# Kernel optimization log

Measured on AMD Instinct MI355X. Metric: run time of the kernel, lower is better.

## Reference

```python
import jax, jax.numpy as jnp
import numpy as np

N_NODES = 100000
N_EDGES = 1600000
N_GRAPHS = 256
NEG_SLOPE_GAT = 0.2   # GATConv default
NEG_SLOPE_ACT = 0.01  # F.leaky_relu default


def _leaky(x, s):
    return jnp.where(x >= 0, x, s * x)


def _gat_layer(x, src, dst, W, a_src, a_dst, b, n):
    # h = W x ; per-node attention logits
    h = x @ W                      # [N, D]
    al_s = h @ a_src               # [N]
    al_d = h @ a_dst               # [N]
    e = _leaky(al_s[src] + al_d[dst], NEG_SLOPE_GAT)  # [E]
    # segment softmax over incoming edges of each dst node
    m = jax.ops.segment_max(e, dst, num_segments=n)
    m = jnp.where(jnp.isfinite(m), m, 0.0)
    ex = jnp.exp(e - m[dst])
    s = jax.ops.segment_sum(ex, dst, num_segments=n)
    alpha = ex / (s[dst] + 1e-16)
    out = jax.ops.segment_sum(h[src] * alpha[:, None], dst, num_segments=n)
    return out + b


def setup_inputs() -> dict:
    key = jax.random.key(0)
    ks = jax.random.split(key, 12)
    x = jax.random.normal(ks[0], (N_NODES, 72), dtype=jnp.float32)
    edge_index = jax.random.randint(ks[1], (2, N_EDGES), 0, N_NODES, dtype=jnp.int64)
    batch = jnp.sort(jax.random.randint(ks[2], (N_NODES,), 0, N_GRAPHS, dtype=jnp.int64))
    def glorot(k, shape):
        fan = shape[0] + shape[-1]
        return jax.random.normal(k, shape, dtype=jnp.float32) * jnp.sqrt(2.0 / fan)
    return {
        "x": x, "edge_index": edge_index, "batch": batch,
        "W1": glorot(ks[3], (72, 64)),
        "a_src1": glorot(ks[4], (64,)), "a_dst1": glorot(ks[5], (64,)),
        "b1": jnp.zeros((64,), jnp.float32),
        "W2": glorot(ks[6], (64, 64)),
        "a_src2": glorot(ks[7], (64,)), "a_dst2": glorot(ks[8], (64,)),
        "b2": jnp.zeros((64,), jnp.float32),
        "fcW": glorot(ks[9], (64, 2)),
        "fcb": jnp.zeros((2,), jnp.float32),
    }


def reference(x, edge_index, batch, W1, a_src1, a_dst1, b1, W2, a_src2, a_dst2, b2, fcW, fcb):
    n = x.shape[0]
    # PyG GATConv adds self-loops by default
    loops = jnp.arange(n, dtype=edge_index.dtype)
    src = jnp.concatenate([edge_index[0], loops])
    dst = jnp.concatenate([edge_index[1], loops])
    h = _gat_layer(x, src, dst, W1, a_src1, a_dst1, b1, n)
    h = _leaky(h, NEG_SLOPE_ACT)
    h = _gat_layer(h, src, dst, W2, a_src2, a_dst2, b2, n)
    # global mean pool over graphs
    sums = jax.ops.segment_sum(h, batch, num_segments=N_GRAPHS)
    cnt = jax.ops.segment_sum(jnp.ones((n,), h.dtype), batch, num_segments=N_GRAPHS)
    pooled = sums / jnp.maximum(cnt, 1.0)[:, None]
    # dropout is identity at inference
    return pooled @ fcW + fcb
```

## Files before the change

### kernel.cpp

```cpp
#include <hip/hip_runtime.h>
#include <hip/hip_bf16.h>
#include <math.h>


#define NPB 256
#define EPB 4096
#define PSTRIDE 4608
#define XPAD 68

__device__ __forceinline__ unsigned int f2bf(float v) {
    unsigned int b = __float_as_uint(v);
    b += 0x7FFFu + ((b >> 16) & 1u);
    return b >> 16;
}

__device__ __forceinline__ int scanIncl256(int v, int t, int* wsum) {
    int lane = t & 63, wv = t >> 6;
#pragma unroll
    for (int o = 1; o < 64; o <<= 1) {
        int u = __shfl_up(v, o);
        if (lane >= o) v += u;
    }
    if (lane == 63) wsum[wv] = v;
    __syncthreads();
    int base = 0;
#pragma unroll
    for (int i = 0; i < 3; i++) base += (i < wv) ? wsum[i] : 0;
    __syncthreads();
    return v + base;
}

struct PartSh {
    int h[512];
    int ls[512];
    int lcur[512];
    int hb[512];
    int s2[256];
    int wsum[4];
    unsigned int Qp[EPB];
    unsigned short Bq[EPB];
};
struct GemmSh {
    float Ws[72 * 64];
    float xs[72][XPAD];
};
union FusedSh { PartSh p; GemmSh g; };

__global__ __launch_bounds__(256) void part_gemm(const int* __restrict__ ei,
                                                 int E, int NB,
                                                 int* __restrict__ bcur,
                                                 unsigned int* __restrict__ pairs,
                                                 int gPart,
                                                 const float* __restrict__ x,
                                                 const float* __restrict__ W,
                                                 const float* __restrict__ a_src,
                                                 const float* __restrict__ a_dst,
                                                 unsigned short* __restrict__ h16,
                                                 float* __restrict__ al_s,
                                                 float* __restrict__ al_d,
                                                 int n) {
    __shared__ FusedSh sh;
    int t = threadIdx.x;
    if ((int)blockIdx.x < gPart) {
        int* h = sh.p.h;
        int* ls = sh.p.ls;
        int* lcur = sh.p.lcur;
        int* hb = sh.p.hb;
        int* s2 = sh.p.s2;
        for (int i = t; i < 512; i += 256) h[i] = 0;
        __syncthreads();
        int i0 = blockIdx.x * EPB;
        unsigned int val[16];
        int bk[16];
        const int4* s4p = (const int4*)(ei);
        const int4* d4p = (const int4*)(ei + E);
#pragma unroll
        for (int k = 0; k < 4; k++) {
            int vbase = (i0 >> 2) + k * 256 + t;
            int i = vbase << 2;
            if (i < E) {
                int4 s4 = s4p[vbase];
                int4 d4 = d4p[vbase];
                int ss[4] = {s4.x, s4.y, s4.z, s4.w};
                int dd[4] = {d4.x, d4.y, d4.z, d4.w};
#pragma unroll
                for (int j = 0; j < 4; j++) {
                    int e = k * 4 + j;
                    bk[e] = dd[j] >> 8;
                    val[e] = (unsigned)ss[j] | ((unsigned)(dd[j] & 255) << 24);
                    atomicAdd(&h[bk[e]], 1);
                }
            } else {
#pragma unroll
                for (int j = 0; j < 4; j++) bk[k * 4 + j] = -1;
            }
        }
        __syncthreads();
        int p0 = h[2 * t], p1 = h[2 * t + 1];
        int incl = scanIncl256(p0 + p1, t, sh.p.wsum);
        s2[t] = incl;
        int ex = incl - p0 - p1;
        ls[2 * t] = ex;           ls[2 * t + 1] = ex + p0;
        lcur[2 * t] = ex;         lcur[2 * t + 1] = ex + p0;
        __syncthreads();
        for (int b = t; b < NB; b += 256)
            hb[b] = h[b] ? atomicAdd(&bcur[b], h[b]) : 0;
        __syncthreads();
#pragma unroll
        for (int e = 0; e < 16; e++) {
            if (bk[e] < 0) continue;
            int pos = atomicAdd(&lcur[bk[e]], 1);
            sh.p.Qp[pos] = val[e];
            sh.p.Bq[pos] = (unsigned short)bk[e];
        }
        __syncthreads();
        int total = s2[255];
        for (int j = t; j < total; j += 256) {
            int bkj = sh.p.Bq[j];
            int gp = hb[bkj] + (j - ls[bkj]);
            if (gp < PSTRIDE)
                pairs[(size_t)bkj * PSTRIDE + gp] = sh.p.Qp[j];
        }
    } else {
        constexpr int IN_DIM = 72;
        float* Ws = sh.g.Ws;
        int nbase = ((int)blockIdx.x - gPart) * 64;

        for (int idx = t; idx < IN_DIM * 16; idx += 256)
            ((float4*)Ws)[idx] = ((const float4*)W)[idx];
        const float* xb = x + (size_t)nbase * IN_DIM;
        int lim = min(64, n - nbase) * IN_DIM;
        constexpr int NV = (64 * IN_DIM) / 4;
        for (int idx = t; idx < NV; idx += 256) {
            int f0 = idx * 4;
            float4 v = make_float4(0.0f, 0.0f, 0.0f, 0.0f);
            if (f0 < lim) v = ((const float4*)xb)[idx];
            int node = f0 / IN_DIM;
            int k = f0 - node * IN_DIM;
            sh.g.xs[k + 0][node] = v.x;
            sh.g.xs[k + 1][node] = v.y;
            sh.g.xs[k + 2][node] = v.z;
            sh.g.xs[k + 3][node] = v.w;
        }
        __syncthreads();

        int cg = t & 15;
        int ng = t >> 4;
        float acc[4][4] = {};
#pragma unroll 8
        for (int k = 0; k < IN_DIM; k++) {
            float4 xv = *(const float4*)&sh.g.xs[k][ng * 4];
            float4 wv = *(const float4*)&Ws[k * 64 + cg * 4];
            float xa[4] = {xv.x, xv.y, xv.z, xv.w};
            float wa[4] = {wv.x, wv.y, wv.z, wv.w};
#pragma unroll
            for (int i = 0; i < 4; i++)
#pragma unroll
                for (int j = 0; j < 4; j++)
                    acc[i][j] += xa[i] * wa[j];
        }

        float4 as4 = *(const float4*)(a_src + cg * 4);
        float4 ad4 = *(const float4*)(a_dst + cg * 4);
#pragma unroll
        for (int i = 0; i < 4; i++) {
            int node = nbase + ng * 4 + i;
            if (node < n) {
                uint2 p;
                p.x = f2bf(acc[i][0]) | (f2bf(acc[i][1]) << 16);
                p.y = f2bf(acc[i][2]) | (f2bf(acc[i][3]) << 16);
                *(uint2*)(h16 + (size_t)node * 64 + cg * 4) = p;
            }
            float vs = acc[i][0] * as4.x + acc[i][1] * as4.y +
                       acc[i][2] * as4.z + acc[i][3] * as4.w;
            float vd = acc[i][0] * ad4.x + acc[i][1] * ad4.y +
                       acc[i][2] * ad4.z + acc[i][3] * ad4.w;
#pragma unroll
            for (int o = 8; o; o >>= 1) {
                vs += __shfl_xor(vs, o);
                vd += __shfl_xor(vd, o);
            }
            if (cg == 0 && node < n) { al_s[node] = vs; al_d[node] = vd; }
        }
    }
}

__global__ __launch_bounds__(256) void build_csr(const unsigned int* __restrict__ pairs,
                                                 const int* __restrict__ bcur,
                                                 int n, int NB,
                                                 int* __restrict__ rowptr,
                                                 int* __restrict__ srcs) {
    int b = blockIdx.x, t = threadIdx.x;
    __shared__ int c[512];
    __shared__ int s2[256];
    __shared__ int wsum[4];
    __shared__ int sbase, stot;
    __shared__ unsigned int Q[PSTRIDE];
    __shared__ int S[NPB + PSTRIDE];
    __shared__ int hist[256];
    __shared__ int hcur[256];
    int c0 = (2 * t < NB) ? min(bcur[2 * t], PSTRIDE) : 0;
    int c1 = (2 * t + 1 < NB) ? min(bcur[2 * t + 1], PSTRIDE) : 0;
    c[2 * t] = c0; c[2 * t + 1] = c1;
    hist[t] = 0;
    __syncthreads();
    int incl = scanIncl256(c0 + c1, t, wsum);
    s2[t] = incl;
    __syncthreads();
    if (t == 0) {
        int p = b >> 1;
        int ex = s2[p] - (c[2 * p] + c[2 * p + 1]);
        sbase = ex + ((b & 1) ? c[b & ~1] : 0);
        stot = s2[255];
    }
    __syncthreads();
    int d0 = b << 8;
    int nb = min(NPB, n - d0);
    int cnt_b = c[b];
    int csr0 = sbase + d0;
    const unsigned int* pb = pairs + (size_t)b * PSTRIDE;

    for (int j = t; j < cnt_b; j += 256)
        atomicAdd(&hist[(pb[j] & 0xFFFFFFu) >> 9], 1);
    __syncthreads();
    int hv = hist[t];
    int hincl = scanIncl256(hv, t, wsum);
    hcur[t] = hincl - hv;
    __syncthreads();
    for (int j = t; j < cnt_b; j += 256) {
        unsigned int p = pb[j];
        int pos = atomicAdd(&hcur[(p & 0xFFFFFFu) >> 9], 1);
        Q[pos] = p;
    }
    __syncthreads();

    __shared__ int deg[NPB];
    __shared__ int cur[NPB];
    deg[t] = (t < nb) ? 1 : 0;
    __syncthreads();
    for (int j = t; j < cnt_b; j += 256)
        atomicAdd(&deg[Q[j] >> 24], 1);
    __syncthreads();
    int v = deg[t];
    int dincl = scanIncl256(v, t, wsum);
    int excl = dincl - v;
    if (t < nb) {
        rowptr[d0 + t] = csr0 + excl;
        S[excl] = d0 + t;
        cur[t] = excl + 1;
    }
    __syncthreads();
    for (int j = t; j < cnt_b; j += 256) {
        unsigned int p = Q[j];
        int off = atomicAdd(&cur[p >> 24], 1);
        S[off] = (int)(p & 0x00FFFFFFu);
    }
    __syncthreads();
    int seg = nb + cnt_b;
    for (int j = t; j < seg; j += 256)
        srcs[csr0 + j] = S[j];
    if (b == 0 && t == 0) rowptr[n] = n + stot;
}

template <int IN_DIM>
__global__ __launch_bounds__(256) void node_gemm(const float* __restrict__ x,
                                                 const float* __restrict__ W,
                                                 const float* __restrict__ a_src,
                                                 const float* __restrict__ a_dst,
                                                 const float* __restrict__ bias_in,
                                                 float slope_in,
                                                 unsigned short* __restrict__ h16,
                                                 float* __restrict__ al_s,
                                                 float* __restrict__ al_d,
                                                 int n) {
    __shared__ float Ws[IN_DIM * 64];
    __shared__ float xs[IN_DIM][XPAD];
    int t = threadIdx.x;
    int nbase = blockIdx.x * 64;

    for (int idx = t; idx < IN_DIM * 16; idx += 256)
        ((float4*)Ws)[idx] = ((const float4*)W)[idx];
    const float* xb = x + (size_t)nbase * IN_DIM;
    int lim = min(64, n - nbase) * IN_DIM;
    constexpr int NV = (64 * IN_DIM) / 4;
    for (int idx = t; idx < NV; idx += 256) {
        int f0 = idx * 4;
        float4 v = make_float4(0.0f, 0.0f, 0.0f, 0.0f);
        if (f0 < lim) v = ((const float4*)xb)[idx];
        int node = f0 / IN_DIM;
        int k = f0 - node * IN_DIM;
        if (bias_in) {
            v.x += bias_in[k + 0];
            v.y += bias_in[k + 1];
            v.z += bias_in[k + 2];
            v.w += bias_in[k + 3];
            v.x = (v.x >= 0.0f) ? v.x : slope_in * v.x;
            v.y = (v.y >= 0.0f) ? v.y : slope_in * v.y;
            v.z = (v.z >= 0.0f) ? v.z : slope_in * v.z;
            v.w = (v.w >= 0.0f) ? v.w : slope_in * v.w;
        }
        xs[k + 0][node] = v.x;
        xs[k + 1][node] = v.y;
        xs[k + 2][node] = v.z;
        xs[k + 3][node] = v.w;
    }
    __syncthreads();

    int cg = t & 15;
    int ng = t >> 4;
    float acc[4][4] = {};
#pragma unroll 8
    for (int k = 0; k < IN_DIM; k++) {
        float4 xv = *(const float4*)&xs[k][ng * 4];
        float4 wv = *(const float4*)&Ws[k * 64 + cg * 4];
        float xa[4] = {xv.x, xv.y, xv.z, xv.w};
        float wa[4] = {wv.x, wv.y, wv.z, wv.w};
#pragma unroll
        for (int i = 0; i < 4; i++)
#pragma unroll
            for (int j = 0; j < 4; j++)
                acc[i][j] += xa[i] * wa[j];
    }

    float4 as4 = *(const float4*)(a_src + cg * 4);
    float4 ad4 = *(const float4*)(a_dst + cg * 4);
#pragma unroll
    for (int i = 0; i < 4; i++) {
        int node = nbase + ng * 4 + i;
        if (node < n) {
            uint2 p;
            p.x = f2bf(acc[i][0]) | (f2bf(acc[i][1]) << 16);
            p.y = f2bf(acc[i][2]) | (f2bf(acc[i][3]) << 16);
            *(uint2*)(h16 + (size_t)node * 64 + cg * 4) = p;
        }
        float vs = acc[i][0] * as4.x + acc[i][1] * as4.y +
                   acc[i][2] * as4.z + acc[i][3] * as4.w;
        float vd = acc[i][0] * ad4.x + acc[i][1] * ad4.y +
                   acc[i][2] * ad4.z + acc[i][3] * ad4.w;
#pragma unroll
        for (int o = 8; o; o >>= 1) {
            vs += __shfl_xor(vs, o);
            vd += __shfl_xor(vd, o);
        }
        if (cg == 0 && node < n) { al_s[node] = vs; al_d[node] = vd; }
    }
}

__device__ __forceinline__ void bf8_fma(float* acc, uint4 q, float w) {
    acc[0] += w * __uint_as_float(q.x << 16);
    acc[1] += w * __uint_as_float(q.x & 0xFFFF0000u);
    acc[2] += w * __uint_as_float(q.y << 16);
    acc[3] += w * __uint_as_float(q.y & 0xFFFF0000u);
    acc[4] += w * __uint_as_float(q.z << 16);
    acc[5] += w * __uint_as_float(q.z & 0xFFFF0000u);
    acc[6] += w * __uint_as_float(q.w << 16);
    acc[7] += w * __uint_as_float(q.w & 0xFFFF0000u);
}

__global__ __launch_bounds__(256) void gat_aggregate(const int* __restrict__ rowptr,
                                                     const int* __restrict__ srcs,
                                                     const float* __restrict__ als,
                                                     const float* __restrict__ ald,
                                                     const unsigned short* __restrict__ h16,
                                                     float* __restrict__ hout,
                                                     int n) {
    int t = threadIdx.x;
    int sub = t >> 3, lane = t & 7;
    int node = blockIdx.x * 32 + sub;
    if (node >= n) return;
    int beg = rowptr[node], end = rowptr[node + 1];
    float aldv = ald[node];
    const unsigned short* hb = h16 + lane * 8;

    float acc[8] = {};
    float sm = 0.0f;
    int j = beg;
    if (j + 4 <= end) {
        int s0 = srcs[j], s1 = srcs[j + 1], s2 = srcs[j + 2], s3 = srcs[j + 3];
        for (; j + 8 <= end; j += 4) {
            int n0 = srcs[j + 4], n1 = srcs[j + 5];
            int n2 = srcs[j + 6], n3 = srcs[j + 7];
            float e0 = als[s0] + aldv, e1 = als[s1] + aldv;
            float e2 = als[s2] + aldv, e3 = als[s3] + aldv;
            uint4 q0 = *(const uint4*)(hb + (size_t)s0 * 64);
            uint4 q1 = *(const uint4*)(hb + (size_t)s1 * 64);
            uint4 q2 = *(const uint4*)(hb + (size_t)s2 * 64);
            uint4 q3 = *(const uint4*)(hb + (size_t)s3 * 64);
            e0 = (e0 >= 0.0f) ? e0 : 0.2f * e0;
            e1 = (e1 >= 0.0f) ? e1 : 0.2f * e1;
            e2 = (e2 >= 0.0f) ? e2 : 0.2f * e2;
            e3 = (e3 >= 0.0f) ? e3 : 0.2f * e3;
            float w0 = __expf(e0), w1 = __expf(e1);
            float w2 = __expf(e2), w3 = __expf(e3);
            sm += (w0 + w1) + (w2 + w3);
            bf8_fma(acc, q0, w0);
            bf8_fma(acc, q1, w1);
            bf8_fma(acc, q2, w2);
            bf8_fma(acc, q3, w3);
            s0 = n0; s1 = n1; s2 = n2; s3 = n3;
        }
        {
            float e0 = als[s0] + aldv, e1 = als[s1] + aldv;
            float e2 = als[s2] + aldv, e3 = als[s3] + aldv;
            uint4 q0 = *(const uint4*)(hb + (size_t)s0 * 64);
            uint4 q1 = *(const uint4*)(hb + (size_t)s1 * 64);
            uint4 q2 = *(const uint4*)(hb + (size_t)s2 * 64);
            uint4 q3 = *(const uint4*)(hb + (size_t)s3 * 64);
            e0 = (e0 >= 0.0f) ? e0 : 0.2f * e0;
            e1 = (e1 >= 0.0f) ? e1 : 0.2f * e1;
            e2 = (e2 >= 0.0f) ? e2 : 0.2f * e2;
            e3 = (e3 >= 0.0f) ? e3 : 0.2f * e3;
            float w0 = __expf(e0), w1 = __expf(e1);
            float w2 = __expf(e2), w3 = __expf(e3);
            sm += (w0 + w1) + (w2 + w3);
            bf8_fma(acc, q0, w0);
            bf8_fma(acc, q1, w1);
            bf8_fma(acc, q2, w2);
            bf8_fma(acc, q3, w3);
            j += 4;
        }
    }
    for (; j < end; j++) {
        int s = srcs[j];
        float e = als[s] + aldv;
        e = (e >= 0.0f) ? e : 0.2f * e;
        float w = __expf(e);
        uint4 q = *(const uint4*)(hb + (size_t)s * 64);
        sm += w;
        bf8_fma(acc, q, w);
    }

    float inv = 1.0f / (sm + 1e-16f);
    float4 o0 = make_float4(acc[0] * inv, acc[1] * inv, acc[2] * inv, acc[3] * inv);
    float4 o1 = make_float4(acc[4] * inv, acc[5] * inv, acc[6] * inv, acc[7] * inv);
    float* op = hout + (size_t)node * 64 + lane * 8;
    *(float4*)op = o0;
    *(float4*)(op + 4) = o1;
}

__global__ __launch_bounds__(256) void pool_fc(const float* __restrict__ hout,
                                               const float* __restrict__ b2,
                                               const int* __restrict__ batch,
                                               const float* __restrict__ fcW,
                                               const float* __restrict__ fcb,
                                               float* __restrict__ out, int n) {
    int g = blockIdx.x;
    int t = threadIdx.x;
    __shared__ int sLo, sHi;
    __shared__ float red[16][64];
    if (t == 0) {
        int lo = 0, hi = n;
        while (lo < hi) { int m = (lo + hi) >> 1; if (batch[m] < g) lo = m + 1; else hi = m; }
        sLo = lo;
    } else if (t == 64) {
        int lo = 0, hi = n;
        while (lo < hi) { int m = (lo + hi) >> 1; if (batch[m] < g + 1) lo = m + 1; else hi = m; }
        sHi = lo;
    }
    __syncthreads();
    int lo = sLo, hi = sHi;
    int q = t & 15;
    int r = t >> 4;
    float4 a4 = make_float4(0.0f, 0.0f, 0.0f, 0.0f);
    for (int node = lo + r; node < hi; node += 16) {
        float4 v = *(const float4*)(hout + (size_t)node * 64 + q * 4);
        a4.x += v.x; a4.y += v.y; a4.z += v.z; a4.w += v.w;
    }
    *(float4*)&red[r][q * 4] = a4;
    __syncthreads();
    if (t < 64) {
        float c = (float)(hi - lo);
        float s = 0.0f;
#pragma unroll
        for (int i = 0; i < 16; i++) s += red[i][t];
        s += c * b2[t];
        float cd = (c > 1.0f) ? c : 1.0f;
        float p = s / cd;
        float s0 = p * fcW[t * 2 + 0];
        float s1 = p * fcW[t * 2 + 1];
#pragma unroll
        for (int o = 32; o; o >>= 1) {
            s0 += __shfl_xor(s0, o);
            s1 += __shfl_xor(s1, o);
        }
        if (t == 0) {
            out[g * 2 + 0] = s0 + fcb[0];
            out[g * 2 + 1] = s1 + fcb[1];
        }
    }
}

extern "C" void kernel_launch(void* const* d_in, const int* in_sizes, int n_in,
                              void* d_out, int out_size, void* d_ws, size_t ws_size,
                              hipStream_t stream) {
    const float* x    = (const float*)d_in[0];
    const int*   ei   = (const int*)d_in[1];
    const int*   batch= (const int*)d_in[2];
    const float* W1   = (const float*)d_in[3];
    const float* as1  = (const float*)d_in[4];
    const float* ad1  = (const float*)d_in[5];
    const float* b1   = (const float*)d_in[6];
    const float* W2   = (const float*)d_in[7];
    const float* as2  = (const float*)d_in[8];
    const float* ad2  = (const float*)d_in[9];
    const float* b2   = (const float*)d_in[10];
    const float* fcW  = (const float*)d_in[11];
    const float* fcb  = (const float*)d_in[12];
    float* out = (float*)d_out;

    const int N = in_sizes[2];
    const int E = in_sizes[1] / 2;
    const int G = out_size / 2;
    const int tot = E + N;
    const int NB = (N + NPB - 1) / NPB;

    float* ws     = (float*)d_ws;
    float* bufO   = ws;
    unsigned int* pairs  = (unsigned int*)bufO;
    float* als    = bufO + (size_t)N * 64;
    float* ald    = als + N;
    int*   rowptr = (int*)(ald + N);
    int*   srcs   = rowptr + N + 1;
    int*   bcur   = srcs + tot;
    unsigned short* bufH16 = (unsigned short*)(bcur + NB);

    dim3 b256(256);
    int gPart = (E + EPB - 1) / EPB;
    int gGemm = (N + 63) / 64;
    int gAgg  = (N + 31) / 32;

    hipMemsetAsync(bcur, 0, (size_t)NB * sizeof(int), stream);
    part_gemm<<<gPart + gGemm, b256, 0, stream>>>(ei, E, NB, bcur, pairs, gPart,
                                                  x, W1, as1, ad1,
                                                  bufH16, als, ald, N);
    build_csr<<<NB, b256, 0, stream>>>(pairs, bcur, N, NB, rowptr, srcs);

    gat_aggregate<<<gAgg, b256, 0, stream>>>(rowptr, srcs, als, ald, bufH16, bufO, N);

    node_gemm<64><<<gGemm, b256, 0, stream>>>(bufO, W2, as2, ad2, b1, 0.01f,
                                              bufH16, als, ald, N);
    gat_aggregate<<<gAgg, b256, 0, stream>>>(rowptr, srcs, als, ald, bufH16, bufO, N);

    pool_fc<<<G, b256, 0, stream>>>(bufO, b2, batch, fcW, fcb, out, N);
}
```

Measured before the change: 287.8 us.

## Fuse layer-1 GEMM with CSR build instead of edge partition kernel

The layer-1 node GEMM blocks move out of the partition kernel and into the CSR-build kernel, which becomes a combined csr_gemm launch. The CSR shared memory is reorganised into a union of phases so it fits alongside the GEMM tiles. The aim is to balance work across the two launches, overlapping the GEMM with the LDS-heavy CSR build rather than with the atomic-heavy partition pass. The trade-off is that csr_gemm's shared-memory footprint is the larger of the two layouts, which may limit occupancy for the GEMM blocks.

```diff
diff --git a/kernel.cpp b/kernel.cpp
--- a/kernel.cpp
+++ b/kernel.cpp
@@ -30,101 +30,168 @@
     return v + base;
 }
 
-struct PartSh {
-    int h[512];
-    int ls[512];
-    int lcur[512];
-    int hb[512];
-    int s2[256];
-    int wsum[4];
-    unsigned int Qp[EPB];
-    unsigned short Bq[EPB];
-};
-struct GemmSh {
-    float Ws[72 * 64];
-    float xs[72][XPAD];
-};
-union FusedSh { PartSh p; GemmSh g; };
-
-__global__ __launch_bounds__(256) void part_gemm(const int* __restrict__ ei,
+__global__ __launch_bounds__(256) void partition(const int* __restrict__ ei,
                                                  int E, int NB,
                                                  int* __restrict__ bcur,
-                                                 unsigned int* __restrict__ pairs,
-                                                 int gPart,
-                                                 const float* __restrict__ x,
-                                                 const float* __restrict__ W,
-                                                 const float* __restrict__ a_src,
-                                                 const float* __restrict__ a_dst,
-                                                 unsigned short* __restrict__ h16,
-                                                 float* __restrict__ al_s,
-                                                 float* __restrict__ al_d,
-                                                 int n) {
-    __shared__ FusedSh sh;
+                                                 unsigned int* __restrict__ pairs) {
+    __shared__ int h[512];
+    __shared__ int ls[512];
+    __shared__ int lcur[512];
+    __shared__ int hb[512];
+    __shared__ int s2[256];
+    __shared__ int wsum[4];
+    __shared__ unsigned int Qp[EPB];
+    __shared__ unsigned short Bq[EPB];
     int t = threadIdx.x;
-    if ((int)blockIdx.x < gPart) {
-        int* h = sh.p.h;
-        int* ls = sh.p.ls;
-        int* lcur = sh.p.lcur;
-        int* hb = sh.p.hb;
-        int* s2 = sh.p.s2;
-        for (int i = t; i < 512; i += 256) h[i] = 0;
-        __syncthreads();
-        int i0 = blockIdx.x * EPB;
-        unsigned int val[16];
-        int bk[16];
-        const int4* s4p = (const int4*)(ei);
-        const int4* d4p = (const int4*)(ei + E);
-#pragma unroll
-        for (int k = 0; k < 4; k++) {
-            int vbase = (i0 >> 2) + k * 256 + t;
-            int i = vbase << 2;
-            if (i < E) {
-                int4 s4 = s4p[vbase];
-                int4 d4 = d4p[vbase];
-                int ss[4] = {s4.x, s4.y, s4.z, s4.w};
-                int dd[4] = {d4.x, d4.y, d4.z, d4.w};
-#pragma unroll
-                for (int j = 0; j < 4; j++) {
-                    int e = k * 4 + j;
-                    bk[e] = dd[j] >> 8;
-                    val[e] = (unsigned)ss[j] | ((unsigned)(dd[j] & 255) << 24);
-                    atomicAdd(&h[bk[e]], 1);
-                }
-            } else {
-#pragma unroll
-                for (int j = 0; j < 4; j++) bk[k * 4 + j] = -1;
+    for (int i = t; i < 512; i += 256) h[i] = 0;
+    __syncthreads();
+    int i0 = blockIdx.x * EPB;
+    unsigned int val[16];
+    int bk[16];
+    const int4* s4p = (const int4*)(ei);
+    const int4* d4p = (const int4*)(ei + E);
+#pragma unroll
+    for (int k = 0; k < 4; k++) {
+        int vbase = (i0 >> 2) + k * 256 + t;
+        int i = vbase << 2;
+        if (i < E) {
+            int4 s4 = s4p[vbase];
+            int4 d4 = d4p[vbase];
+            int ss[4] = {s4.x, s4.y, s4.z, s4.w};
+            int dd[4] = {d4.x, d4.y, d4.z, d4.w};
+#pragma unroll
+            for (int j = 0; j < 4; j++) {
+                int e = k * 4 + j;
+                bk[e] = dd[j] >> 8;
+                val[e] = (unsigned)ss[j] | ((unsigned)(dd[j] & 255) << 24);
+                atomicAdd(&h[bk[e]], 1);
             }
-        }
-        __syncthreads();
-        int p0 = h[2 * t], p1 = h[2 * t + 1];
-        int incl = scanIncl256(p0 + p1, t, sh.p.wsum);
-        s2[t] = incl;
-        int ex = incl - p0 - p1;
-        ls[2 * t] = ex;           ls[2 * t + 1] = ex + p0;
-        lcur[2 * t] = ex;         lcur[2 * t + 1] = ex + p0;
-        __syncthreads();
-        for (int b = t; b < NB; b += 256)
-            hb[b] = h[b] ? atomicAdd(&bcur[b], h[b]) : 0;
-        __syncthreads();
-#pragma unroll
-        for (int e = 0; e < 16; e++) {
-            if (bk[e] < 0) continue;
-            int pos = atomicAdd(&lcur[bk[e]], 1);
-            sh.p.Qp[pos] = val[e];
-            sh.p.Bq[pos] = (unsigned short)bk[e];
-        }
-        __syncthreads();
-        int total = s2[255];
-        for (int j = t; j < total; j += 256) {
-            int bkj = sh.p.Bq[j];
-            int gp = hb[bkj] + (j - ls[bkj]);
-            if (gp < PSTRIDE)
-                pairs[(size_t)bkj * PSTRIDE + gp] = sh.p.Qp[j];
-        }
+        } else {
+#pragma unroll
+            for (int j = 0; j < 4; j++) bk[k * 4 + j] = -1;
+        }
+    }
+    __syncthreads();
+    int p0 = h[2 * t], p1 = h[2 * t + 1];
+    int incl = scanIncl256(p0 + p1, t, wsum);
+    s2[t] = incl;
+    int ex = incl - p0 - p1;
+    ls[2 * t] = ex;           ls[2 * t + 1] = ex + p0;
+    lcur[2 * t] = ex;         lcur[2 * t + 1] = ex + p0;
+    __syncthreads();
+    for (int b = t; b < NB; b += 256)
+        hb[b] = h[b] ? atomicAdd(&bcur[b], h[b]) : 0;
+    __syncthreads();
+#pragma unroll
+    for (int e = 0; e < 16; e++) {
+        if (bk[e] < 0) continue;
+        int pos = atomicAdd(&lcur[bk[e]], 1);
+        Qp[pos] = val[e];
+        Bq[pos] = (unsigned short)bk[e];
+    }
+    __syncthreads();
+    int total = s2[255];
+    for (int j = t; j < total; j += 256) {
+        int bkj = Bq[j];
+        int gp = hb[bkj] + (j - ls[bkj]);
+        if (gp < PSTRIDE)
+            pairs[(size_t)bkj * PSTRIDE + gp] = Qp[j];
+    }
+}
+
+struct CsrP1 { int c[512]; int s2[256]; };
+struct CsrP2 { int hist[256]; int hcur[256]; };
+struct CsrP3 { int deg[NPB]; int cur[NPB]; int S[NPB + PSTRIDE]; };
+struct CsrSh {
+    unsigned int Q[PSTRIDE];
+    union { CsrP1 p1; CsrP2 p2; CsrP3 p3; } u;
+    int wsum[4];
+    int sbase, stot;
+};
+struct GemmSh72 { float Ws[72 * 64]; float xs[72][XPAD]; };
+union CsrGemmSh { CsrSh c; GemmSh72 g; };
+
+__global__ __launch_bounds__(256) void csr_gemm(const unsigned int* __restrict__ pairs,
+                                                const int* __restrict__ bcur,
+                                                int n, int NB,
+                                                int* __restrict__ rowptr,
+                                                int* __restrict__ srcs,
+                                                const float* __restrict__ x,
+                                                const float* __restrict__ W,
+                                                const float* __restrict__ a_src,
+                                                const float* __restrict__ a_dst,
+                                                unsigned short* __restrict__ h16,
+                                                float* __restrict__ al_s,
+                                                float* __restrict__ al_d) {
+    __shared__ CsrGemmSh sh;
+    int t = threadIdx.x;
+    if ((int)blockIdx.x < NB) {
+        int b = blockIdx.x;
+        int c0 = (2 * t < NB) ? min(bcur[2 * t], PSTRIDE) : 0;
+        int c1 = (2 * t + 1 < NB) ? min(bcur[2 * t + 1], PSTRIDE) : 0;
+        sh.c.u.p1.c[2 * t] = c0; sh.c.u.p1.c[2 * t + 1] = c1;
+        __syncthreads();
+        int incl = scanIncl256(c0 + c1, t, sh.c.wsum);
+        sh.c.u.p1.s2[t] = incl;
+        __syncthreads();
+        if (t == 0) {
+            int p = b >> 1;
+            int ex = sh.c.u.p1.s2[p] - (sh.c.u.p1.c[2 * p] + sh.c.u.p1.c[2 * p + 1]);
+            sh.c.sbase = ex + ((b & 1) ? sh.c.u.p1.c[b & ~1] : 0);
+            sh.c.stot = sh.c.u.p1.s2[255];
+        }
+        __syncthreads();
+        int d0 = b << 8;
+        int nb = min(NPB, n - d0);
+        int cnt_b = sh.c.u.p1.c[b];
+        int csr0 = sh.c.sbase + d0;
+        const unsigned int* pb = pairs + (size_t)b * PSTRIDE;
+        __syncthreads();
+
+        sh.c.u.p2.hist[t] = 0;
+        __syncthreads();
+        for (int j = t; j < cnt_b; j += 256)
+            atomicAdd(&sh.c.u.p2.hist[(pb[j] & 0xFFFFFFu) >> 9], 1);
+        __syncthreads();
+        int hv = sh.c.u.p2.hist[t];
+        int hincl = scanIncl256(hv, t, sh.c.wsum);
+        sh.c.u.p2.hcur[t] = hincl - hv;
+        __syncthreads();
+        for (int j = t; j < cnt_b; j += 256) {
+            unsigned int p = pb[j];
+            int pos = atomicAdd(&sh.c.u.p2.hcur[(p & 0xFFFFFFu) >> 9], 1);
+            sh.c.Q[pos] = p;
+        }
+        __syncthreads();
+
+        sh.c.u.p3.deg[t] = (t < nb) ? 1 : 0;
+        __syncthreads();
+        for (int j = t; j < cnt_b; j += 256)
+            atomicAdd(&sh.c.u.p3.deg[sh.c.Q[j] >> 24], 1);
+        __syncthreads();
+        int v = sh.c.u.p3.deg[t];
+        int dincl = scanIncl256(v, t, sh.c.wsum);
+        int excl = dincl - v;
+        if (t < nb) {
+            rowptr[d0 + t] = csr0 + excl;
+            sh.c.u.p3.S[excl] = d0 + t;
+            sh.c.u.p3.cur[t] = excl + 1;
+        }
+        __syncthreads();
+        for (int j = t; j < cnt_b; j += 256) {
+            unsigned int p = sh.c.Q[j];
+            int off = atomicAdd(&sh.c.u.p3.cur[p >> 24], 1);
+            sh.c.u.p3.S[off] = (int)(p & 0x00FFFFFFu);
+        }
+        __syncthreads();
+        int seg = nb + cnt_b;
+        for (int j = t; j < seg; j += 256)
+            srcs[csr0 + j] = sh.c.u.p3.S[j];
+        if (b == 0 && t == 0) rowptr[n] = n + sh.c.stot;
     } else {
         constexpr int IN_DIM = 72;
         float* Ws = sh.g.Ws;
-        int nbase = ((int)blockIdx.x - gPart) * 64;
+        int nbase = ((int)blockIdx.x - NB) * 64;
 
         for (int idx = t; idx < IN_DIM * 16; idx += 256)
             ((float4*)Ws)[idx] = ((const float4*)W)[idx];
@@ -183,83 +250,6 @@
             if (cg == 0 && node < n) { al_s[node] = vs; al_d[node] = vd; }
         }
     }
-}
-
-__global__ __launch_bounds__(256) void build_csr(const unsigned int* __restrict__ pairs,
-                                                 const int* __restrict__ bcur,
-                                                 int n, int NB,
-                                                 int* __restrict__ rowptr,
-                                                 int* __restrict__ srcs) {
-    int b = blockIdx.x, t = threadIdx.x;
-    __shared__ int c[512];
-    __shared__ int s2[256];
-    __shared__ int wsum[4];
-    __shared__ int sbase, stot;
-    __shared__ unsigned int Q[PSTRIDE];
-    __shared__ int S[NPB + PSTRIDE];
-    __shared__ int hist[256];
-    __shared__ int hcur[256];
-    int c0 = (2 * t < NB) ? min(bcur[2 * t], PSTRIDE) : 0;
-    int c1 = (2 * t + 1 < NB) ? min(bcur[2 * t + 1], PSTRIDE) : 0;
-    c[2 * t] = c0; c[2 * t + 1] = c1;
-    hist[t] = 0;
-    __syncthreads();
-    int incl = scanIncl256(c0 + c1, t, wsum);
-    s2[t] = incl;
-    __syncthreads();
-    if (t == 0) {
-        int p = b >> 1;
-        int ex = s2[p] - (c[2 * p] + c[2 * p + 1]);
-        sbase = ex + ((b & 1) ? c[b & ~1] : 0);
-        stot = s2[255];
-    }
-    __syncthreads();
-    int d0 = b << 8;
-    int nb = min(NPB, n - d0);
-    int cnt_b = c[b];
-    int csr0 = sbase + d0;
-    const unsigned int* pb = pairs + (size_t)b * PSTRIDE;
-
-    for (int j = t; j < cnt_b; j += 256)
-        atomicAdd(&hist[(pb[j] & 0xFFFFFFu) >> 9], 1);
-    __syncthreads();
-    int hv = hist[t];
-    int hincl = scanIncl256(hv, t, wsum);
-    hcur[t] = hincl - hv;
-    __syncthreads();
-    for (int j = t; j < cnt_b; j += 256) {
-        unsigned int p = pb[j];
-        int pos = atomicAdd(&hcur[(p & 0xFFFFFFu) >> 9], 1);
-        Q[pos] = p;
-    }
-    __syncthreads();
-
-    __shared__ int deg[NPB];
-    __shared__ int cur[NPB];
-    deg[t] = (t < nb) ? 1 : 0;
-    __syncthreads();
-    for (int j = t; j < cnt_b; j += 256)
-        atomicAdd(&deg[Q[j] >> 24], 1);
-    __syncthreads();
-    int v = deg[t];
-    int dincl = scanIncl256(v, t, wsum);
-    int excl = dincl - v;
-    if (t < nb) {
-        rowptr[d0 + t] = csr0 + excl;
-        S[excl] = d0 + t;
-        cur[t] = excl + 1;
-    }
-    __syncthreads();
-    for (int j = t; j < cnt_b; j += 256) {
-        unsigned int p = Q[j];
-        int off = atomicAdd(&cur[p >> 24], 1);
-        S[off] = (int)(p & 0x00FFFFFFu);
-    }
-    __syncthreads();
-    int seg = nb + cnt_b;
-    for (int j = t; j < seg; j += 256)
-        srcs[csr0 + j] = S[j];
-    if (b == 0 && t == 0) rowptr[n] = n + stot;
 }
 
 template <int IN_DIM>
@@ -530,10 +520,10 @@
     int gAgg  = (N + 31) / 32;
 
     hipMemsetAsync(bcur, 0, (size_t)NB * sizeof(int), stream);
-    part_gemm<<<gPart + gGemm, b256, 0, stream>>>(ei, E, NB, bcur, pairs, gPart,
-                                                  x, W1, as1, ad1,
-                                                  bufH16, als, ald, N);
-    build_csr<<<NB, b256, 0, stream>>>(pairs, bcur, N, NB, rowptr, srcs);
+    partition<<<gPart, b256, 0, stream>>>(ei, E, NB, bcur, pairs);
+    csr_gemm<<<NB + gGemm, b256, 0, stream>>>(pairs, bcur, N, NB, rowptr, srcs,
+                                              x, W1, as1, ad1,
+                                              bufH16, als, ald);
 
     gat_aggregate<<<gAgg, b256, 0, stream>>>(rowptr, srcs, als, ald, bufH16, bufO, N);
 
```

Result: no change. 285.5 us (-0.8%).
